# Performance work log

Hardware: AMD Instinct MI355X
Metric: run time of the kernel (lower is better)

The kernel has to match this reference:

```python
import jax, jax.numpy as jnp
import numpy as np

B, H, D = 1024, 4096, 65536

def setup_inputs() -> dict:
    key = jax.random.key(0)
    k1, k2, k3, k4 = jax.random.split(key, 4)
    x = jax.random.normal(k1, (B, H), dtype=jnp.float32)
    W_enc = jax.random.normal(k2, (D, H), dtype=jnp.float32) * (1.0 / np.sqrt(H))
    b_enc = jax.random.normal(k3, (D,), dtype=jnp.float32) * 0.01
    W_dec = jax.random.normal(k4, (H, D), dtype=jnp.float32)
    # match torch init: decoder columns normalized along dim=0
    W_dec = W_dec / jnp.linalg.norm(W_dec, axis=0, keepdims=True)
    pre_bias = jnp.zeros((H,), dtype=jnp.float32)
    return {"x": x, "W_enc": W_enc, "b_enc": b_enc, "W_dec": W_dec,
            "pre_bias": pre_bias, "k": 64}

def reference(x, W_enc, b_enc, W_dec, pre_bias, k):
    # encode: center, linear, top-k, relu on kept values
    x_centered = x - pre_bias                      # [B, H]
    pre_act = x_centered @ W_enc.T + b_enc         # [B, D]
    top_vals, top_idx = jax.lax.top_k(pre_act, k)  # [B, k], [B, k]
    top_vals = jax.nn.relu(top_vals)
    # decode: scatter k values into dense dictionary vector, then GEMM
    rows = jnp.arange(pre_act.shape[0])[:, None]   # [B, 1]
    sparse = jnp.zeros(pre_act.shape, dtype=top_vals.dtype).at[rows, top_idx].set(top_vals)
    x_hat = sparse @ W_dec.T + pre_bias            # [B, H]
    return x_hat, top_vals, top_idx, pre_act
```

## Files before the change

kernel.cpp:

```cpp
#include <hip/hip_runtime.h>
#include <hip/hip_bf16.h>
#include <cstdint>
#include <cstddef>
#include <math.h>

#define B_DIM 1024
#define H_DIM 4096
#define D_DIM 65536
#define K_TOP 64
#define CAND_CAP 512
#define RECOMP 96
#define RECOMP_PAD 128
#define COLLECT_THRESH 2.8f

typedef float f32x4 __attribute__((ext_vector_type(4)));
typedef __bf16 bf16x8 __attribute__((ext_vector_type(8)));
typedef unsigned short u16x8 __attribute__((ext_vector_type(8)));

__device__ inline unsigned short f2bf(float f) {
    unsigned int u = __float_as_uint(f);
    unsigned int r = u + 0x7FFFu + ((u >> 16) & 1u);
    return (unsigned short)(r >> 16);
}
__device__ inline float bf2f(unsigned short s) {
    return __uint_as_float(((unsigned int)s) << 16);
}
__device__ inline unsigned int pk2bf(float a, float b) {
    __hip_bfloat162 h = __float22bfloat162_rn(make_float2(a, b));
    return *reinterpret_cast<unsigned int*>(&h);
}

__global__ void convert_x_kernel(const float* __restrict__ x,
                                 const float* __restrict__ pre_bias,
                                 unsigned short* __restrict__ xc) {
    int i = blockIdx.x * blockDim.x + threadIdx.x;
    float4 v = *(const float4*)&x[(size_t)i * 4];
    int h = (i * 4) & (H_DIM - 1);
    float4 pb = *(const float4*)&pre_bias[h];
    ushort4 o;
    o.x = f2bf(v.x - pb.x);
    o.y = f2bf(v.y - pb.y);
    o.z = f2bf(v.z - pb.z);
    o.w = f2bf(v.w - pb.w);
    *(ushort4*)&xc[(size_t)i * 4] = o;
}

#define N_BM 128
#define N_BN 128
#define N_BK 64
#define NGEMM_BLK ((B_DIM / N_BM) * (D_DIM / N_BN))

__global__ void __launch_bounds__(256, 3) gemm_enc_fused_kernel(
        const unsigned short* __restrict__ A,
        const float* __restrict__ Wenc,
        const float* __restrict__ b_enc,
        float* __restrict__ pre_act,
        int* __restrict__ cnt,
        int* __restrict__ cidx,
        float* __restrict__ cval) {
    __shared__ __align__(16) unsigned short sA[N_BM * N_BK];
    __shared__ __align__(16) unsigned short sB[N_BN * N_BK];

    const int tid = threadIdx.x;
    const int w = tid >> 6;
    const int l = tid & 63;
    const int bid = blockIdx.x;
    const int m0 = (((bid >> 3) & 7)) * N_BM;
    const int n0 = ((bid & 7) * 64 + (bid >> 6)) * N_BN;
    const int wm = w >> 1, wn = w & 1;
    const int lrow8 = l >> 3, lseg = l & 7;
    const int sw_seg = lseg ^ lrow8;

    f32x4 acc[4][4] = {};

    for (int k0 = 0; k0 < H_DIM; k0 += N_BK) {
        #pragma unroll
        for (int i = 0; i < 4; i++) {
            int rbase = w * 32 + i * 8;
            const unsigned short* src = &A[(size_t)(m0 + rbase + lrow8) * H_DIM + k0 + sw_seg * 8];
            __builtin_amdgcn_global_load_lds(
                (const __attribute__((address_space(1))) unsigned int*)src,
                (__attribute__((address_space(3))) unsigned int*)&sA[rbase * N_BK],
                16, 0, 0);
        }
        #pragma unroll
        for (int i = 0; i < 4; i++) {
            int row = w * 32 + i * 8 + lrow8;
            const float* src = &Wenc[(size_t)(n0 + row) * H_DIM + k0 + lseg * 8];
            float4 f0 = *(const float4*)src;
            float4 f1 = *(const float4*)(src + 4);
            uint4 o;
            o.x = pk2bf(f0.x, f0.y);
            o.y = pk2bf(f0.z, f0.w);
            o.z = pk2bf(f1.x, f1.y);
            o.w = pk2bf(f1.z, f1.w);
            *(uint4*)&sB[row * N_BK + sw_seg * 8] = o;
        }
        __syncthreads();

        #pragma unroll
        for (int ks = 0; ks < 2; ks++) {
            const int slot = ks * 4 + (l >> 4);
            const int rslot = (slot ^ (l & 7)) * 8;
            bf16x8 bfr[4];
            #pragma unroll
            for (int nj = 0; nj < 4; nj++) {
                int r = wn * 64 + nj * 16 + (l & 15);
                bfr[nj] = *(bf16x8*)&sB[r * N_BK + rslot];
            }
            #pragma unroll
            for (int mi = 0; mi < 4; mi++) {
                int r = wm * 64 + mi * 16 + (l & 15);
                bf16x8 afr = *(bf16x8*)&sA[r * N_BK + rslot];
                #pragma unroll
                for (int nj = 0; nj < 4; nj++)
                    acc[mi][nj] = __builtin_amdgcn_mfma_f32_16x16x32_bf16(afr, bfr[nj], acc[mi][nj], 0, 0, 0);
            }
        }
        __syncthreads();
    }

    const int lc = l & 15, lr4 = (l >> 4) * 4;
    #pragma unroll
    for (int nj = 0; nj < 4; nj++) {
        int col = n0 + wn * 64 + nj * 16 + lc;
        float bias = b_enc[col];
        #pragma unroll
        for (int mi = 0; mi < 4; mi++) {
            int row = m0 + wm * 64 + mi * 16 + lr4;
            #pragma unroll
            for (int e = 0; e < 4; e++) {
                float v = acc[mi][nj][e] + bias;
                pre_act[(size_t)(row + e) * D_DIM + col] = v;
                if (v > COLLECT_THRESH) {
                    int b = row + e;
                    int p = atomicAdd(&cnt[b], 1);
                    if (p < CAND_CAP) {
                        cidx[b * CAND_CAP + p] = col;
                        cval[b * CAND_CAP + p] = v;
                    }
                }
            }
        }
    }
}

__global__ void __launch_bounds__(256) transpose_wdec_kernel(
        const float* __restrict__ Wdec, unsigned short* __restrict__ WdecT) {
    __shared__ float tile[64][65];
    const int d0 = blockIdx.x * 64;
    const int h0 = blockIdx.y * 64;
    const int tc = threadIdx.x & 63, tr = threadIdx.x >> 6;
    #pragma unroll
    for (int hh = tr; hh < 64; hh += 4)
        tile[hh][tc] = Wdec[(size_t)(h0 + hh) * D_DIM + d0 + tc];
    __syncthreads();
    #pragma unroll
    for (int dd = tr; dd < 64; dd += 4)
        WdecT[(size_t)(d0 + dd) * H_DIM + h0 + tc] = f2bf(tile[tc][dd]);
}

__global__ void __launch_bounds__(256) select_decode_kernel(
        const float* __restrict__ x, const float* __restrict__ pre_bias,
        const float* __restrict__ Wenc, const float* __restrict__ b_enc,
        const int* __restrict__ cnt, const int* __restrict__ cidx, const float* __restrict__ cval,
        const unsigned short* __restrict__ WdecT,
        float* __restrict__ out_vals, float* __restrict__ out_idx,
        float* __restrict__ x_hat) {
    __shared__ float s_val[CAND_CAP];
    __shared__ int   s_idx[CAND_CAP];
    __shared__ __align__(16) float s_x[H_DIM];
    __shared__ double s_dv[RECOMP_PAD];
    __shared__ int    s_di[RECOMP_PAD];
    __shared__ float  s_v2[K_TOP];
    __shared__ int    s_d2[K_TOP];

    const int b = blockIdx.x;
    const int tid = threadIdx.x;

    for (int i = tid; i < H_DIM / 4; i += 256) {
        float4 xv = *(const float4*)&x[(size_t)b * H_DIM + i * 4];
        float4 pb = *(const float4*)&pre_bias[i * 4];
        xv.x -= pb.x; xv.y -= pb.y; xv.z -= pb.z; xv.w -= pb.w;
        *(float4*)&s_x[i * 4] = xv;
    }
    const int n = min(cnt[b], CAND_CAP);
    for (int i = tid; i < CAND_CAP; i += 256) {
        if (i < n) { s_val[i] = cval[b * CAND_CAP + i]; s_idx[i] = cidx[b * CAND_CAP + i]; }
        else       { s_val[i] = -1e30f;                 s_idx[i] = 0x7FFFFFFF; }
    }
    __syncthreads();

    for (int k = 2; k <= CAND_CAP; k <<= 1) {
        for (int j = k >> 1; j > 0; j >>= 1) {
            int p = tid;
            int i1 = (p / j) * 2 * j + (p % j);
            int i2 = i1 + j;
            bool up = ((i1 & k) == 0);
            float v1 = s_val[i1], v2 = s_val[i2];
            int  d1 = s_idx[i1],  d2 = s_idx[i2];
            bool before12 = (v1 > v2) || (v1 == v2 && d1 < d2);
            bool before21 = (v2 > v1) || (v2 == v1 && d2 < d1);
            bool sw = up ? before21 : before12;
            __syncthreads();
            if (sw) { s_val[i1] = v2; s_val[i2] = v1; s_idx[i1] = d2; s_idx[i2] = d1; }
            __syncthreads();
        }
    }

    const int T = min(RECOMP, n);
    double dv = -1e300;
    int di = 0x7FFFFFFF;
    if (tid < T) {
        di = s_idx[tid];
        const float* wr = &Wenc[(size_t)di * H_DIM];
        double a0 = 0, a1 = 0, a2 = 0, a3 = 0;
        for (int h = 0; h < H_DIM; h += 4) {
            float4 wv = *(const float4*)&wr[h];
            float4 xv = *(const float4*)&s_x[h];
            a0 += (double)xv.x * (double)wv.x;
            a1 += (double)xv.y * (double)wv.y;
            a2 += (double)xv.z * (double)wv.z;
            a3 += (double)xv.w * (double)wv.w;
        }
        dv = ((a0 + a1) + (a2 + a3)) + (double)b_enc[di];
    }
    __syncthreads();
    if (tid < RECOMP_PAD) { s_dv[tid] = (tid < T) ? dv : -1e300; s_di[tid] = di; }

    for (int k = 2; k <= RECOMP_PAD; k <<= 1) {
        for (int j = k >> 1; j > 0; j >>= 1) {
            __syncthreads();
            if (tid < RECOMP_PAD / 2) {
                int p = tid;
                int i1 = (p / j) * 2 * j + (p % j);
                int i2 = i1 + j;
                bool up = ((i1 & k) == 0);
                double v1 = s_dv[i1], v2 = s_dv[i2];
                int  d1 = s_di[i1],  d2 = s_di[i2];
                bool before12 = (v1 > v2) || (v1 == v2 && d1 < d2);
                bool before21 = (v2 > v1) || (v2 == v1 && d2 < d1);
                bool sw = up ? before21 : before12;
                if (sw) { s_dv[i1] = v2; s_dv[i2] = v1; s_di[i1] = d2; s_di[i2] = d1; }
            }
        }
    }
    __syncthreads();
    if (tid < K_TOP) {
        double v = s_dv[tid];
        float rv = (float)(v > 0.0 ? v : 0.0);
        out_vals[b * K_TOP + tid] = rv;
        out_idx[b * K_TOP + tid]  = (float)s_di[tid];
        s_v2[tid] = rv;
        s_d2[tid] = s_di[tid];
    }
    __syncthreads();

    const int t = tid;
    float acc[16] = {};
    #pragma unroll 4
    for (int j = 0; j < K_TOP; j++) {
        float v = s_v2[j];
        const unsigned short* wr = &WdecT[(size_t)s_d2[j] * H_DIM];
        u16x8 w0 = *(const u16x8*)&wr[t * 8];
        u16x8 w1 = *(const u16x8*)&wr[2048 + t * 8];
        #pragma unroll
        for (int e = 0; e < 8; e++) {
            acc[e]     = fmaf(v, bf2f(w0[e]), acc[e]);
            acc[8 + e] = fmaf(v, bf2f(w1[e]), acc[8 + e]);
        }
    }
    #pragma unroll
    for (int c = 0; c < 2; c++) {
        int h = c * 2048 + t * 8;
        float4 pb0 = *(const float4*)&pre_bias[h];
        float4 pb1 = *(const float4*)&pre_bias[h + 4];
        float4 o0, o1;
        o0.x = acc[c*8+0] + pb0.x; o0.y = acc[c*8+1] + pb0.y;
        o0.z = acc[c*8+2] + pb0.z; o0.w = acc[c*8+3] + pb0.w;
        o1.x = acc[c*8+4] + pb1.x; o1.y = acc[c*8+5] + pb1.y;
        o1.z = acc[c*8+6] + pb1.z; o1.w = acc[c*8+7] + pb1.w;
        *(float4*)&x_hat[(size_t)b * H_DIM + h]     = o0;
        *(float4*)&x_hat[(size_t)b * H_DIM + h + 4] = o1;
    }
}

#define G_BM 256
#define G_BN 128
#define G_BK 64

__global__ void __launch_bounds__(256) gemm_enc_kernel(
        const unsigned short* __restrict__ A,
        const float* __restrict__ Wenc,
        const float* __restrict__ b_enc,
        float* __restrict__ pre_act) {
    __shared__ __align__(16) unsigned short sA[G_BM * G_BK];
    __shared__ __align__(16) unsigned short sB[G_BN * G_BK];

    const int tid = threadIdx.x;
    const int w = tid >> 6;
    const int l = tid & 63;
    const int m0 = blockIdx.x * G_BM;
    const int n0 = blockIdx.y * G_BN;
    const int wm = w >> 1, wn = w & 1;
    const int lrow8 = l >> 3, lseg = l & 7;
    const int sw_seg = lseg ^ lrow8;

    f32x4 acc[8][4] = {};

    for (int k0 = 0; k0 < H_DIM; k0 += G_BK) {
        #pragma unroll
        for (int i = 0; i < 8; i++) {
            int row = w * 64 + i * 8 + lrow8;
            const unsigned short* src = &A[(size_t)(m0 + row) * H_DIM + k0 + sw_seg * 8];
            __builtin_amdgcn_global_load_lds(
                (const __attribute__((address_space(1))) unsigned int*)src,
                (__attribute__((address_space(3))) unsigned int*)&sA[(w * 64 + i * 8) * G_BK],
                16, 0, 0);
        }
        #pragma unroll
        for (int i = 0; i < 4; i++) {
            int row = w * 32 + i * 8 + lrow8;
            const float* src = &Wenc[(size_t)(n0 + row) * H_DIM + k0 + lseg * 8];
            float4 f0 = *(const float4*)src;
            float4 f1 = *(const float4*)(src + 4);
            u16x8 o;
            o[0] = f2bf(f0.x); o[1] = f2bf(f0.y); o[2] = f2bf(f0.z); o[3] = f2bf(f0.w);
            o[4] = f2bf(f1.x); o[5] = f2bf(f1.y); o[6] = f2bf(f1.z); o[7] = f2bf(f1.w);
            *(u16x8*)&sB[row * G_BK + sw_seg * 8] = o;
        }
        __syncthreads();

        #pragma unroll
        for (int ks = 0; ks < 2; ks++) {
            const int slot = ks * 4 + (l >> 4);
            const int rslot = (slot ^ (l & 7)) * 8;
            bf16x8 bfr[4];
            #pragma unroll
            for (int nj = 0; nj < 4; nj++) {
                int r = wn * 64 + nj * 16 + (l & 15);
                bfr[nj] = *(bf16x8*)&sB[r * G_BK + rslot];
            }
            #pragma unroll
            for (int mi = 0; mi < 8; mi++) {
                int r = wm * 128 + mi * 16 + (l & 15);
                bf16x8 afr = *(bf16x8*)&sA[r * G_BK + rslot];
                #pragma unroll
                for (int nj = 0; nj < 4; nj++)
                    acc[mi][nj] = __builtin_amdgcn_mfma_f32_16x16x32_bf16(afr, bfr[nj], acc[mi][nj], 0, 0, 0);
            }
        }
        __syncthreads();
    }

    const int lc = l & 15, lr4 = (l >> 4) * 4;
    #pragma unroll
    for (int nj = 0; nj < 4; nj++) {
        int col = n0 + wn * 64 + nj * 16 + lc;
        float bias = b_enc[col];
        #pragma unroll
        for (int mi = 0; mi < 8; mi++) {
            int row = m0 + wm * 128 + mi * 16 + lr4;
            #pragma unroll
            for (int e = 0; e < 4; e++) {
                pre_act[(size_t)(row + e) * D_DIM + col] = acc[mi][nj][e] + bias;
            }
        }
    }
}

__global__ void collect_kernel(const float* __restrict__ pre_act,
                               int* __restrict__ cnt,
                               int* __restrict__ cidx,
                               float* __restrict__ cval) {
    int i = blockIdx.x * blockDim.x + threadIdx.x;
    float4 v = *(const float4*)&pre_act[(size_t)i * 4];
    float fv[4] = {v.x, v.y, v.z, v.w};
    int base = i * 4;
    #pragma unroll
    for (int e = 0; e < 4; e++) {
        if (fv[e] > COLLECT_THRESH) {
            int idx = base + e;
            int b = idx >> 16;
            int d = idx & (D_DIM - 1);
            int p = atomicAdd(&cnt[b], 1);
            if (p < CAND_CAP) {
                cidx[b * CAND_CAP + p] = d;
                cval[b * CAND_CAP + p] = fv[e];
            }
        }
    }
}

__global__ void __launch_bounds__(256) select_topk_kernel(
        const float* __restrict__ x, const float* __restrict__ pre_bias,
        const float* __restrict__ Wenc, const float* __restrict__ b_enc,
        const int* __restrict__ cnt, const int* __restrict__ cidx, const float* __restrict__ cval,
        float* __restrict__ out_vals, float* __restrict__ out_idx) {
    __shared__ float s_val[CAND_CAP];
    __shared__ int   s_idx[CAND_CAP];
    __shared__ __align__(16) float s_x[H_DIM];
    __shared__ double s_dv[RECOMP_PAD];
    __shared__ int    s_di[RECOMP_PAD];

    const int b = blockIdx.x;
    const int tid = threadIdx.x;

    for (int i = tid; i < H_DIM / 4; i += 256) {
        float4 xv = *(const float4*)&x[(size_t)b * H_DIM + i * 4];
        float4 pb = *(const float4*)&pre_bias[i * 4];
        xv.x -= pb.x; xv.y -= pb.y; xv.z -= pb.z; xv.w -= pb.w;
        *(float4*)&s_x[i * 4] = xv;
    }
    const int n = min(cnt[b], CAND_CAP);
    for (int i = tid; i < CAND_CAP; i += 256) {
        if (i < n) { s_val[i] = cval[b * CAND_CAP + i]; s_idx[i] = cidx[b * CAND_CAP + i]; }
        else       { s_val[i] = -1e30f;                 s_idx[i] = 0x7FFFFFFF; }
    }
    __syncthreads();

    for (int k = 2; k <= CAND_CAP; k <<= 1) {
        for (int j = k >> 1; j > 0; j >>= 1) {
            int p = tid;
            int i1 = (p / j) * 2 * j + (p % j);
            int i2 = i1 + j;
            bool up = ((i1 & k) == 0);
            float v1 = s_val[i1], v2 = s_val[i2];
            int  d1 = s_idx[i1],  d2 = s_idx[i2];
            bool before12 = (v1 > v2) || (v1 == v2 && d1 < d2);
            bool before21 = (v2 > v1) || (v2 == v1 && d2 < d1);
            bool sw = up ? before21 : before12;
            __syncthreads();
            if (sw) { s_val[i1] = v2; s_val[i2] = v1; s_idx[i1] = d2; s_idx[i2] = d1; }
            __syncthreads();
        }
    }

    const int T = min(RECOMP, n);
    double dv = -1e300;
    int di = 0x7FFFFFFF;
    if (tid < T) {
        di = s_idx[tid];
        const float* wr = &Wenc[(size_t)di * H_DIM];
        double a0 = 0, a1 = 0, a2 = 0, a3 = 0;
        for (int h = 0; h < H_DIM; h += 4) {
            float4 wv = *(const float4*)&wr[h];
            float4 xv = *(const float4*)&s_x[h];
            a0 += (double)xv.x * (double)wv.x;
            a1 += (double)xv.y * (double)wv.y;
            a2 += (double)xv.z * (double)wv.z;
            a3 += (double)xv.w * (double)wv.w;
        }
        dv = ((a0 + a1) + (a2 + a3)) + (double)b_enc[di];
    }
    __syncthreads();
    if (tid < RECOMP_PAD) { s_dv[tid] = (tid < T) ? dv : -1e300; s_di[tid] = di; }

    for (int k = 2; k <= RECOMP_PAD; k <<= 1) {
        for (int j = k >> 1; j > 0; j >>= 1) {
            __syncthreads();
            if (tid < RECOMP_PAD / 2) {
                int p = tid;
                int i1 = (p / j) * 2 * j + (p % j);
                int i2 = i1 + j;
                bool up = ((i1 & k) == 0);
                double v1 = s_dv[i1], v2 = s_dv[i2];
                int  d1 = s_di[i1],  d2 = s_di[i2];
                bool before12 = (v1 > v2) || (v1 == v2 && d1 < d2);
                bool before21 = (v2 > v1) || (v2 == v1 && d2 < d1);
                bool sw = up ? before21 : before12;
                if (sw) { s_dv[i1] = v2; s_dv[i2] = v1; s_di[i1] = d2; s_di[i2] = d1; }
            }
        }
    }
    __syncthreads();
    if (tid < K_TOP) {
        double v = s_dv[tid];
        out_vals[b * K_TOP + tid] = (float)(v > 0.0 ? v : 0.0);
        out_idx[b * K_TOP + tid]  = (float)s_di[tid];
    }
}

__global__ void __launch_bounds__(64) decode_kernel(
        const float* __restrict__ out_vals,
        const float* __restrict__ out_idx,
        const float* __restrict__ Wdec,
        const float* __restrict__ pre_bias,
        float* __restrict__ x_hat_t) {
    __shared__ float2 s_vi[64 * 64];
    const int lane = threadIdx.x;
    const int s0 = (blockIdx.x >> 3) & 15;

    for (int i = lane; i < 64 * 64; i += 64) {
        int j = i >> 6, bb = i & 63;
        int b = s0 * 64 + bb;
        float v = out_vals[b * K_TOP + j];
        int id = (int)out_idx[b * K_TOP + j];
        s_vi[i] = make_float2(v, __int_as_float(id << 2));
    }
    __syncthreads();

    const int b = s0 * 64 + lane;
    for (int wi = blockIdx.x; wi < H_DIM * 16; wi += 1280) {
        const int h = (wi & 7) + ((wi >> 7) << 3);
        const char* wr = (const char*)(Wdec + (size_t)h * D_DIM);
        float acc = 0.0f;
        #pragma unroll 8
        for (int j = 0; j < K_TOP; j++) {
            float2 vi = s_vi[j * 64 + lane];
            acc = fmaf(vi.x, *(const float*)(wr + __float_as_int(vi.y)), acc);
        }
        x_hat_t[(size_t)h * B_DIM + b] = acc + pre_bias[h];
    }
}

__global__ void __launch_bounds__(256) transpose_kernel(const float* __restrict__ xt,
                                                        float* __restrict__ x_hat) {
    __shared__ float tile[64][65];
    const int hb = blockIdx.x * 64;
    const int bb = blockIdx.y * 64;
    const int tc = threadIdx.x & 63, tr = threadIdx.x >> 6;
    #pragma unroll
    for (int r = tr; r < 64; r += 4)
        tile[r][tc] = xt[(size_t)(hb + r) * B_DIM + bb + tc];
    __syncthreads();
    #pragma unroll
    for (int r = tr; r < 64; r += 4)
        x_hat[(size_t)(bb + r) * H_DIM + hb + tc] = tile[tc][r];
}

extern "C" void kernel_launch(void* const* d_in, const int* in_sizes, int n_in,
                              void* d_out, int out_size, void* d_ws, size_t ws_size,
                              hipStream_t stream) {
    const float* x        = (const float*)d_in[0];
    const float* W_enc    = (const float*)d_in[1];
    const float* b_enc    = (const float*)d_in[2];
    const float* W_dec    = (const float*)d_in[3];
    const float* pre_bias = (const float*)d_in[4];

    float* out = (float*)d_out;
    float* x_hat    = out;
    float* top_vals = out + (size_t)B_DIM * H_DIM;
    float* top_idx  = top_vals + (size_t)B_DIM * K_TOP;
    float* pre_act  = top_idx + (size_t)B_DIM * K_TOP;

    unsigned short* xc = (unsigned short*)d_ws;
    int*   cidx  = (int*)((char*)d_ws + (size_t)B_DIM * H_DIM * 2);
    float* cval  = (float*)((char*)cidx + (size_t)B_DIM * CAND_CAP * 4);
    int*   cnt   = (int*)((char*)cval + (size_t)B_DIM * CAND_CAP * 4);
    float* xhatt = (float*)((char*)cnt + 4096);
    const size_t WDT_OFF = 32ull << 20;
    unsigned short* wdecT = (unsigned short*)((char*)d_ws + WDT_OFF);
    const bool big_ws = ws_size >= WDT_OFF + ((size_t)D_DIM * H_DIM * 2) + (1 << 20);

    hipMemsetAsync(cnt, 0, B_DIM * sizeof(int), stream);

    convert_x_kernel<<<(B_DIM * H_DIM / 4) / 256, 256, 0, stream>>>(x, pre_bias, xc);

    if (big_ws) {
        gemm_enc_fused_kernel<<<NGEMM_BLK, 256, 0, stream>>>(
            xc, W_enc, b_enc, pre_act, cnt, cidx, cval);
        dim3 wtgrid(D_DIM / 64, H_DIM / 64);
        transpose_wdec_kernel<<<wtgrid, 256, 0, stream>>>(W_dec, wdecT);
        select_decode_kernel<<<B_DIM, 256, 0, stream>>>(
            x, pre_bias, W_enc, b_enc, cnt, cidx, cval, wdecT,
            top_vals, top_idx, x_hat);
    } else {
        dim3 ggrid(B_DIM / G_BM, D_DIM / G_BN);
        gemm_enc_kernel<<<ggrid, 256, 0, stream>>>(xc, W_enc, b_enc, pre_act);
        collect_kernel<<<(B_DIM * (D_DIM / 4)) / 256, 256, 0, stream>>>(pre_act, cnt, cidx, cval);
        select_topk_kernel<<<B_DIM, 256, 0, stream>>>(x, pre_bias, W_enc, b_enc, cnt, cidx, cval,
                                                      top_vals, top_idx);
        decode_kernel<<<1280, 64, 0, stream>>>(top_vals, top_idx, W_dec, pre_bias, xhatt);
        dim3 tgrid(H_DIM / 64, B_DIM / 64);
        transpose_kernel<<<tgrid, 256, 0, stream>>>(xhatt, x_hat);
    }
}
```

Before: 1.553 ms.

## Rewrite encoder GEMM as 256x256 triple-buffered async-LDS pipeline

The encoder GEMM moves from a 128x128x64 single-buffered tile to a 256x256x32 tile with 512 threads and three LDS stages. Both the bf16 activations and the raw fp32 W_enc are loaded with global_load_lds, and W_enc is converted to bf16 at fragment-read time instead of during staging. The goal is to overlap global loads with MFMA work and raise reuse per loaded byte. In exchange the kernel needs more LDS and more accumulator registers (8x4 fragments per wave), the conversion is redone by every wave that reads a B fragment, and the manual vmcnt/barrier scheme is fragile.

```diff
diff --git a/kernel.cpp b/kernel.cpp
--- a/kernel.cpp
+++ b/kernel.cpp
@@ -45,12 +45,13 @@
     *(ushort4*)&xc[(size_t)i * 4] = o;
 }
 
-#define N_BM 128
-#define N_BN 128
-#define N_BK 64
-#define NGEMM_BLK ((B_DIM / N_BM) * (D_DIM / N_BN))
-
-__global__ void __launch_bounds__(256, 3) gemm_enc_fused_kernel(
+#define P_BM 256
+#define P_BN 256
+#define P_BK 32
+#define P_NK (H_DIM / P_BK)
+#define P_GRID ((B_DIM / P_BM) * (D_DIM / P_BN))
+
+__global__ void __launch_bounds__(512, 2) gemm_enc_pipe256_kernel(
         const unsigned short* __restrict__ A,
         const float* __restrict__ Wenc,
         const float* __restrict__ b_enc,
@@ -58,67 +59,89 @@
         int* __restrict__ cnt,
         int* __restrict__ cidx,
         float* __restrict__ cval) {
-    __shared__ __align__(16) unsigned short sA[N_BM * N_BK];
-    __shared__ __align__(16) unsigned short sB[N_BN * N_BK];
+    __shared__ __align__(16) unsigned short sA[3][P_BM * P_BK];
+    __shared__ __align__(16) float          sB[3][P_BN * P_BK];
 
     const int tid = threadIdx.x;
     const int w = tid >> 6;
     const int l = tid & 63;
     const int bid = blockIdx.x;
-    const int m0 = (((bid >> 3) & 7)) * N_BM;
-    const int n0 = ((bid & 7) * 64 + (bid >> 6)) * N_BN;
-    const int wm = w >> 1, wn = w & 1;
-    const int lrow8 = l >> 3, lseg = l & 7;
-    const int sw_seg = lseg ^ lrow8;
-
-    f32x4 acc[4][4] = {};
-
-    for (int k0 = 0; k0 < H_DIM; k0 += N_BK) {
-        #pragma unroll
-        for (int i = 0; i < 4; i++) {
-            int rbase = w * 32 + i * 8;
-            const unsigned short* src = &A[(size_t)(m0 + rbase + lrow8) * H_DIM + k0 + sw_seg * 8];
-            __builtin_amdgcn_global_load_lds(
-                (const __attribute__((address_space(1))) unsigned int*)src,
-                (__attribute__((address_space(3))) unsigned int*)&sA[rbase * N_BK],
-                16, 0, 0);
-        }
-        #pragma unroll
-        for (int i = 0; i < 4; i++) {
-            int row = w * 32 + i * 8 + lrow8;
-            const float* src = &Wenc[(size_t)(n0 + row) * H_DIM + k0 + lseg * 8];
-            float4 f0 = *(const float4*)src;
-            float4 f1 = *(const float4*)(src + 4);
-            uint4 o;
-            o.x = pk2bf(f0.x, f0.y);
-            o.y = pk2bf(f0.z, f0.w);
-            o.z = pk2bf(f1.x, f1.y);
-            o.w = pk2bf(f1.z, f1.w);
-            *(uint4*)&sB[row * N_BK + sw_seg * 8] = o;
-        }
-        __syncthreads();
-
-        #pragma unroll
-        for (int ks = 0; ks < 2; ks++) {
-            const int slot = ks * 4 + (l >> 4);
-            const int rslot = (slot ^ (l & 7)) * 8;
-            bf16x8 bfr[4];
-            #pragma unroll
-            for (int nj = 0; nj < 4; nj++) {
-                int r = wn * 64 + nj * 16 + (l & 15);
-                bfr[nj] = *(bf16x8*)&sB[r * N_BK + rslot];
-            }
-            #pragma unroll
-            for (int mi = 0; mi < 4; mi++) {
-                int r = wm * 64 + mi * 16 + (l & 15);
-                bf16x8 afr = *(bf16x8*)&sA[r * N_BK + rslot];
-                #pragma unroll
-                for (int nj = 0; nj < 4; nj++)
-                    acc[mi][nj] = __builtin_amdgcn_mfma_f32_16x16x32_bf16(afr, bfr[nj], acc[mi][nj], 0, 0, 0);
-            }
-        }
-        __syncthreads();
-    }
+    const int m0 = ((bid >> 3) & 3) * P_BM;
+    const int n0 = ((bid & 7) * 32 + (bid >> 5)) * P_BN;
+    const int wm = w >> 2, wn = w & 3;
+
+#define P_STAGE(slot, kt) do {                                                          \
+        const int k0_ = (kt) * P_BK;                                                    \
+        _Pragma("unroll")                                                               \
+        for (int j_ = 0; j_ < 2; j_++) {                                                \
+            int r_ = j_ * 128 + w * 16 + (l >> 2);                \
+            const unsigned short* s_ =                                                  \
+                &A[(size_t)(m0 + r_) * H_DIM + k0_ + (((l & 3) ^ ((l >> 2) & 3)) * 8)]; \
+            __builtin_amdgcn_global_load_lds(                                           \
+                (const __attribute__((address_space(1))) unsigned int*)s_,              \
+                (__attribute__((address_space(3))) unsigned int*)                       \
+                    &sA[slot][(j_ * 128 + w * 16) * P_BK],                              \
+                16, 0, 0);                                                              \
+        }                                                                               \
+        _Pragma("unroll")                                                               \
+        for (int j_ = 0; j_ < 4; j_++) {                                                \
+            int r_ = j_ * 64 + w * 8 + (l >> 3);                  \
+            const float* s_ =                                                           \
+                &Wenc[(size_t)(n0 + r_) * H_DIM + k0_ + (((l & 7) ^ ((l >> 3) & 7)) * 4)]; \
+            __builtin_amdgcn_global_load_lds(                                           \
+                (const __attribute__((address_space(1))) unsigned int*)s_,              \
+                (__attribute__((address_space(3))) unsigned int*)                       \
+                    &sB[slot][(j_ * 64 + w * 8) * P_BK],                                \
+                16, 0, 0);                                                              \
+        }                                                                               \
+    } while (0)
+
+#define P_COMPUTE(slot) do {                                                            \
+        bf16x8 bfr_[4];                                                                 \
+        _Pragma("unroll")                                                               \
+        for (int nj_ = 0; nj_ < 4; nj_++) {                                             \
+            int r_ = wn * 64 + nj_ * 16 + (l & 15);                    \
+            int h_ = (l >> 4) * 2;                                                      \
+            f32x4 b0_ = *(const f32x4*)&sB[slot][r_ * P_BK + (((h_    ) ^ (l & 7)) * 4)]; \
+            f32x4 b1_ = *(const f32x4*)&sB[slot][r_ * P_BK + (((h_ + 1) ^ (l & 7)) * 4)]; \
+            union { uint4 u; bf16x8 v; } cv_;                                           \
+            cv_.u.x = pk2bf(b0_[0], b0_[1]); cv_.u.y = pk2bf(b0_[2], b0_[3]);           \
+            cv_.u.z = pk2bf(b1_[0], b1_[1]); cv_.u.w = pk2bf(b1_[2], b1_[3]);           \
+            bfr_[nj_] = cv_.v;                                                          \
+        }                                                                               \
+        _Pragma("unroll")                                                               \
+        for (int mi_ = 0; mi_ < 8; mi_++) {                                             \
+            int r_ = wm * 128 + mi_ * 16 + (l & 15);                   \
+            bf16x8 afr_ = *(const bf16x8*)&sA[slot][r_ * P_BK + (((l >> 4) ^ (l & 3)) * 8)]; \
+            _Pragma("unroll")                                                           \
+            for (int nj_ = 0; nj_ < 4; nj_++)                                           \
+                acc[mi_][nj_] = __builtin_amdgcn_mfma_f32_16x16x32_bf16(                \
+                    afr_, bfr_[nj_], acc[mi_][nj_], 0, 0, 0);                           \
+        }                                                                               \
+    } while (0)
+
+    f32x4 acc[8][4] = {};
+
+    P_STAGE(0, 0);
+    P_STAGE(1, 1);
+
+    int cs = 0;
+    int ws = 2;
+    for (int t = 0; t < P_NK; t++) {
+        int kt = t + 2; if (kt > P_NK - 1) kt = P_NK - 1;
+        P_STAGE(ws, kt);
+        asm volatile("s_waitcnt vmcnt(12)" ::: "memory");
+        __builtin_amdgcn_s_barrier();
+        P_COMPUTE(cs);
+        asm volatile("s_waitcnt lgkmcnt(0)" ::: "memory");
+        __builtin_amdgcn_s_barrier();
+        cs = (cs == 2) ? 0 : cs + 1;
+        ws = (ws == 2) ? 0 : ws + 1;
+    }
+    asm volatile("s_waitcnt vmcnt(0)" ::: "memory");
+
+#undef P_STAGE
+#undef P_COMPUTE
 
     const int lc = l & 15, lr4 = (l >> 4) * 4;
     #pragma unroll
@@ -126,8 +149,8 @@
         int col = n0 + wn * 64 + nj * 16 + lc;
         float bias = b_enc[col];
         #pragma unroll
-        for (int mi = 0; mi < 4; mi++) {
-            int row = m0 + wm * 64 + mi * 16 + lr4;
+        for (int mi = 0; mi < 8; mi++) {
+            int row = m0 + wm * 128 + mi * 16 + lr4;
             #pragma unroll
             for (int e = 0; e < 4; e++) {
                 float v = acc[mi][nj][e] + bias;
@@ -558,7 +581,7 @@
     convert_x_kernel<<<(B_DIM * H_DIM / 4) / 256, 256, 0, stream>>>(x, pre_bias, xc);
 
     if (big_ws) {
-        gemm_enc_fused_kernel<<<NGEMM_BLK, 256, 0, stream>>>(
+        gemm_enc_pipe256_kernel<<<P_GRID, 512, 0, stream>>>(
             xc, W_enc, b_enc, pre_act, cnt, cidx, cval);
         dim3 wtgrid(D_DIM / 64, H_DIM / 64);
         transpose_wdec_kernel<<<wtgrid, 256, 0, stream>>>(W_dec, wdecT);
```

Result: slower. 1.865 ms (+20.1%).
